# Optimization experiments

Hardware: AMD Instinct MI355X
Metric: run time of the kernel (lower is better)

The kernel has to match this reference:

```python
import jax, jax.numpy as jnp
import numpy as np

HEADS = 2
NEG_SLOPE = 0.2
EPS = 1e-16


def setup_inputs() -> dict:
    N, E, D, F = 10000, 320000, 128, 16
    key = jax.random.key(0)
    ks = jax.random.split(key, 8)
    return {
        "x": jax.random.normal(ks[0], (N, D), dtype=jnp.float32),
        "edge_index": jax.random.randint(ks[1], (2, E), 0, N, dtype=jnp.int64),
        "edge_attr": jax.random.normal(ks[2], (E, F), dtype=jnp.float32),
        # stacked per-layer params (5 layers), glorot-ish scale
        "weights": jax.random.normal(ks[3], (5, D, HEADS * D), dtype=jnp.float32) * 0.08,
        "atts": jax.random.normal(ks[4], (5, HEADS, 2 * D), dtype=jnp.float32) * 0.08,
        "biases": jnp.zeros((5, D), dtype=jnp.float32),
        "edge_ws": jax.random.normal(ks[5], (5, HEADS * D, F), dtype=jnp.float32) * 0.2,
        "edge_bs": jnp.zeros((5, HEADS * D), dtype=jnp.float32),
    }


def _gat_layer(x, src, dst, edge_attr_full, W, att, b, ew, eb):
    # x: [N, D]; src/dst: [E_tot] (self loops already appended)
    N, D = x.shape
    H = HEADS
    edge_emb = edge_attr_full @ ew.T + eb               # [E_tot, H*D]
    xw = x @ W                                          # [N, H*D]
    xj = xw[src].reshape(-1, H, D) + edge_emb.reshape(-1, H, D)  # [E_tot, H, D]
    xi = xw[dst].reshape(-1, H, D)
    att_i, att_j = att[:, :D], att[:, D:]               # [H, D] each
    alpha = jnp.einsum('ehd,hd->eh', xi, att_i) + jnp.einsum('ehd,hd->eh', xj, att_j)
    alpha = jax.nn.leaky_relu(alpha, NEG_SLOPE)
    # segment softmax over destination node (every node has a self loop)
    amax = jax.ops.segment_max(alpha, dst, num_segments=N)   # [N, H]
    ea = jnp.exp(alpha - amax[dst])
    denom = jax.ops.segment_sum(ea, dst, num_segments=N)     # [N, H]
    alpha = ea / (denom[dst] + EPS)
    msg = xj * alpha[..., None]                              # [E_tot, H, D]
    aggr = jax.ops.segment_sum(msg, dst, num_segments=N)     # [N, H, D]
    return aggr.mean(axis=1) + b                             # [N, D]


def reference(x, edge_index, edge_attr, weights, atts, biases, edge_ws, edge_bs):
    N = x.shape[0]
    E = edge_index.shape[1]
    F = edge_attr.shape[1]
    # add self loops (PyG flow: edge_index[0]=source j, edge_index[1]=target i)
    loop = jnp.arange(N, dtype=edge_index.dtype)
    src = jnp.concatenate([edge_index[0], loop])
    dst = jnp.concatenate([edge_index[1], loop])
    edge_attr_full = jnp.concatenate(
        [edge_attr, jnp.zeros((N, F), dtype=edge_attr.dtype)], axis=0)
    h = x
    for l in range(5):
        h = _gat_layer(h, src, dst, edge_attr_full,
                       weights[l], atts[l], biases[l], edge_ws[l], edge_bs[l])
        if l < 4:
            h = jax.nn.relu(h)
    return h
```

## Files before the change

### kernel.cpp

```cpp
#include <hip/hip_runtime.h>
#include <hip/hip_fp16.h>
#include <hip/hip_fp8.h>

#define HEADS 2
#define DD 128
#define FF 16
#define HD 256
#define NEG_SLOPE 0.2f
#define EPSV 1e-16f
#define BB 8

typedef float v2f __attribute__((ext_vector_type(2)));

static __device__ __forceinline__ float rdlanef(float v, int i){
  return __uint_as_float(__builtin_amdgcn_readlane(__float_as_uint(v), i));
}
static __device__ __forceinline__ int rdlanei(int v, int i){
  return __builtin_amdgcn_readlane(v, i);
}
static __device__ __forceinline__ float4 h4f(uint2 u){
  float2 f0 = __half22float2(*(__half2*)&u.x);
  float2 f1 = __half22float2(*(__half2*)&u.y);
  return make_float4(f0.x, f0.y, f1.x, f1.y);
}
static __device__ __forceinline__ float4 fp8x4_to_f4(unsigned u){
#if __has_builtin(__builtin_amdgcn_cvt_pk_f32_fp8)
  v2f lo = __builtin_amdgcn_cvt_pk_f32_fp8(u, false);
  v2f hi = __builtin_amdgcn_cvt_pk_f32_fp8(u, true);
  return make_float4(lo.x, lo.y, hi.x, hi.y);
#else
  __hip_fp8_e4m3 b0, b1, b2, b3;
  b0.__x = (unsigned char)(u & 0xff);
  b1.__x = (unsigned char)((u >> 8) & 0xff);
  b2.__x = (unsigned char)((u >> 16) & 0xff);
  b3.__x = (unsigned char)((u >> 24) & 0xff);
  return make_float4((float)b0, (float)b1, (float)b2, (float)b3);
#endif
}

__global__ void k_hist_prec(const int* __restrict__ dst, int* __restrict__ counts,
                            const float* __restrict__ atts, const float* __restrict__ edge_ws,
                            const float* __restrict__ edge_bs, const float* __restrict__ weights,
                            float* __restrict__ c5, __half* __restrict__ wh,
                            int E, int Etot, int ebl){
  int bid = blockIdx.x;
  if (bid >= ebl){
    int k = bid - ebl;
    if (k < 5){
      int l = k, t = threadIdx.x;
      const float* att = atts    + (size_t)l*HEADS*2*DD;
      const float* ew  = edge_ws + (size_t)l*HD*FF;
      const float* eb  = edge_bs + (size_t)l*HD;
      float* c = c5 + (size_t)l*34;
      if (t < 32){
        int h = t >> 4, f = t & 15;
        float acc = 0.f;
        for (int d = 0; d < DD; d++) acc += att[h*2*DD + DD + d]*ew[(size_t)(h*DD+d)*FF + f];
        c[h*FF + f] = acc;
      } else if (t < 34){
        int h = t - 32;
        float acc = 0.f;
        for (int d = 0; d < DD; d++) acc += att[h*2*DD + DD + d]*eb[h*DD + d];
        c[32 + h] = acc;
      }
    } else {
      int base = (k - 5)*1024 + threadIdx.x*4;
      float4 w = *(const float4*)&weights[base];
      __half2 p0 = __floats2half2_rn(w.x, w.y);
      __half2 p1 = __floats2half2_rn(w.z, w.w);
      uint2 pk; pk.x = *(unsigned*)&p0; pk.y = *(unsigned*)&p1;
      *(uint2*)&wh[base] = pk;
    }
    return;
  }
  int e = bid*256 + threadIdx.x;
  if (e >= Etot) return;
  int dn = (e < E) ? dst[e] : (e - E);
  atomicAdd(&counts[dn], 1);
}

__global__ __launch_bounds__(1024) void k_scan(const int* __restrict__ counts, int* __restrict__ starts,
                       int* __restrict__ cursor, int N, int Etot){
  __shared__ int s[1024];
  int t = threadIdx.x;
  const int CHN = (N + 1023) / 1024;
  int lo = t*CHN, hi = min(lo+CHN, N);
  int loc = 0;
  for (int i = lo; i < hi; i++) loc += counts[i];
  s[t] = loc;
  __syncthreads();
  for (int off = 1; off < 1024; off <<= 1){
    int v = (t >= off) ? s[t-off] : 0;
    __syncthreads();
    s[t] += v;
    __syncthreads();
  }
  int run = (t == 0) ? 0 : s[t-1];
  for (int i = lo; i < hi; i++){
    starts[i] = run; cursor[i] = run; run += counts[i];
  }
  if (t == 0) starts[N] = Etot;
}

__global__ void k_scatter(const int* __restrict__ dst, int* __restrict__ cursor,
                          int* __restrict__ eids, int E, int Etot){
  int e = blockIdx.x*256 + threadIdx.x;
  if (e >= Etot) return;
  int dn = (e < E) ? dst[e] : (e - E);
  int pos = atomicAdd(&cursor[dn], 1);
  eids[pos] = e;
}

__global__ void k_gather_csr(const int* __restrict__ eids, const int* __restrict__ src,
                             const float* __restrict__ eattr, const float* __restrict__ c5,
                             int* __restrict__ srcC, __half* __restrict__ attrC16,
                             float* __restrict__ attrdot, int E, int Etot){
  int i = blockIdx.x*256 + threadIdx.x;
  if (i >= Etot) return;
  int eid = eids[i];
  float a[FF];
  if (eid < E){
    srcC[i] = src[eid];
    const float4* in = (const float4*)&eattr[(size_t)eid*FF];
    float4 q0=in[0], q1=in[1], q2=in[2], q3=in[3];
    a[0]=q0.x; a[1]=q0.y; a[2]=q0.z; a[3]=q0.w;
    a[4]=q1.x; a[5]=q1.y; a[6]=q1.z; a[7]=q1.w;
    a[8]=q2.x; a[9]=q2.y; a[10]=q2.z; a[11]=q2.w;
    a[12]=q3.x; a[13]=q3.y; a[14]=q3.z; a[15]=q3.w;
  } else {
    srcC[i] = eid - E;
    #pragma unroll
    for (int f = 0; f < FF; f++) a[f] = 0.f;
  }
  uint4 pk0, pk1;
  {
    __half2 h0 = __floats2half2_rn(a[0],a[1]),  h1 = __floats2half2_rn(a[2],a[3]);
    __half2 h2 = __floats2half2_rn(a[4],a[5]),  h3 = __floats2half2_rn(a[6],a[7]);
    __half2 h4 = __floats2half2_rn(a[8],a[9]),  h5 = __floats2half2_rn(a[10],a[11]);
    __half2 h6 = __floats2half2_rn(a[12],a[13]),h7 = __floats2half2_rn(a[14],a[15]);
    pk0.x=*(unsigned*)&h0; pk0.y=*(unsigned*)&h1; pk0.z=*(unsigned*)&h2; pk0.w=*(unsigned*)&h3;
    pk1.x=*(unsigned*)&h4; pk1.y=*(unsigned*)&h5; pk1.z=*(unsigned*)&h6; pk1.w=*(unsigned*)&h7;
  }
  uint4* ob = (uint4*)&attrC16[(size_t)i*FF];
  ob[0] = pk0; ob[1] = pk1;
  #pragma unroll
  for (int l = 0; l < 5; l++){
    const float* cl = c5 + (size_t)l*34;
    float d0 = 0.f, d1 = 0.f;
    #pragma unroll
    for (int f = 0; f < FF; f++){
      d0 = fmaf(a[f], cl[f], d0);
      d1 = fmaf(a[f], cl[FF+f], d1);
    }
    *(float2*)&attrdot[((size_t)l*Etot + i)*2] = make_float2(d0, d1);
  }
}

__global__ __launch_bounds__(256) void k_gemm_xw(const float* __restrict__ h, const __half* __restrict__ Wh,
                         const float* __restrict__ att, unsigned char* __restrict__ xw8,
                         float* __restrict__ sbuf, int N){
  __shared__ float sx[16][DD];
  int r0 = blockIdx.x * 16;
  int rows = min(16, N - r0);
  int t = threadIdx.x;
  for (int idx = t; idx < 16*(DD/4); idx += 256){
    int r = idx >> 5, kq = idx & 31;
    float4 v = make_float4(0.f,0.f,0.f,0.f);
    if (r < rows) v = *(const float4*)&h[(size_t)(r0+r)*DD + kq*4];
    *(float4*)&sx[r][kq*4] = v;
  }
  __syncthreads();
  int tx = t & 63, ty = t >> 6;
  int c0 = tx*4;
  float4 acc[4];
  #pragma unroll
  for (int r = 0; r < 4; r++) acc[r] = make_float4(0.f,0.f,0.f,0.f);
  #pragma unroll 4
  for (int kq = 0; kq < 32; kq++){
    float4 w0 = h4f(*(const uint2*)&Wh[(size_t)(kq*4+0)*HD + c0]);
    float4 w1 = h4f(*(const uint2*)&Wh[(size_t)(kq*4+1)*HD + c0]);
    float4 w2 = h4f(*(const uint2*)&Wh[(size_t)(kq*4+2)*HD + c0]);
    float4 w3 = h4f(*(const uint2*)&Wh[(size_t)(kq*4+3)*HD + c0]);
    #pragma unroll
    for (int r = 0; r < 4; r++){
      float4 hv = *(const float4*)&sx[ty*4+r][kq*4];
      acc[r].x = fmaf(hv.x, w0.x, acc[r].x); acc[r].y = fmaf(hv.x, w0.y, acc[r].y);
      acc[r].z = fmaf(hv.x, w0.z, acc[r].z); acc[r].w = fmaf(hv.x, w0.w, acc[r].w);
      acc[r].x = fmaf(hv.y, w1.x, acc[r].x); acc[r].y = fmaf(hv.y, w1.y, acc[r].y);
      acc[r].z = fmaf(hv.y, w1.z, acc[r].z); acc[r].w = fmaf(hv.y, w1.w, acc[r].w);
      acc[r].x = fmaf(hv.z, w2.x, acc[r].x); acc[r].y = fmaf(hv.z, w2.y, acc[r].y);
      acc[r].z = fmaf(hv.z, w2.z, acc[r].z); acc[r].w = fmaf(hv.z, w2.w, acc[r].w);
      acc[r].x = fmaf(hv.w, w3.x, acc[r].x); acc[r].y = fmaf(hv.w, w3.y, acc[r].y);
      acc[r].z = fmaf(hv.w, w3.z, acc[r].z); acc[r].w = fmaf(hv.w, w3.w, acc[r].w);
    }
  }
  #pragma unroll
  for (int r = 0; r < 4; r++){
    if (ty*4+r < rows){
      __hip_fp8_e4m3 q0(acc[r].x), q1(acc[r].y), q2(acc[r].z), q3(acc[r].w);
      unsigned pk = (unsigned)q0.__x | ((unsigned)q1.__x << 8)
                  | ((unsigned)q2.__x << 16) | ((unsigned)q3.__x << 24);
      *(unsigned*)&xw8[(size_t)(r0+ty*4+r)*HD + c0] = pk;
    }
  }
  int hsel = tx >> 5;
  int cm = c0 & 127;
  float4 ai = *(const float4*)&att[hsel*2*DD + cm];
  float4 aj = *(const float4*)&att[hsel*2*DD + DD + cm];
  #pragma unroll
  for (int r = 0; r < 4; r++){
    float pi = acc[r].x*ai.x + acc[r].y*ai.y + acc[r].z*ai.z + acc[r].w*ai.w;
    float pj = acc[r].x*aj.x + acc[r].y*aj.y + acc[r].z*aj.z + acc[r].w*aj.w;
    #pragma unroll
    for (int off = 16; off; off >>= 1){
      pi += __shfl_xor(pi, off);
      pj += __shfl_xor(pj, off);
    }
    int row = ty*4 + r;
    if ((tx & 31) == 0 && row < rows){
      sbuf[(size_t)(r0+row)*4 + 0 + hsel] = pi;
      sbuf[(size_t)(r0+row)*4 + 2 + hsel] = pj;
    }
  }
}

__global__ __launch_bounds__(128, 8) void k_aggr(const int* __restrict__ starts, const int* __restrict__ srcC,
                      const __half* __restrict__ attrC16, const float* __restrict__ adL,
                      const float* __restrict__ s, const float* __restrict__ c,
                      const unsigned char* __restrict__ xw8, const float* __restrict__ ew,
                      const float* __restrict__ eb, const float* __restrict__ bias,
                      float* __restrict__ out, int N, int relu){
  int lane = threadIdx.x & 63, wid = threadIdx.x >> 6;
  int n = blockIdx.x*2 + wid;
  if (n >= N) return;

  float c32 = c[32], c33 = c[33];
  float sdx = s[(size_t)n*4+0], sdy = s[(size_t)n*4+1];
  int st = starts[n];
  int deg = starts[n+1] - st;

  int f2 = lane & 15;
  int h2 = (lane >> 4) & 1;
  int hq = lane >> 5;
  const unsigned char* xbase = xw8 + lane*4;

  float aAx=0.f, aAy=0.f, aAz=0.f, aAw=0.f;
  float aBx=0.f, aBy=0.f, aBz=0.f, aBw=0.f;
  float ls0=0.f, ls1=0.f, taccA=0.f, taccB=0.f;

  for (int base = 0; base < deg; base += 64){
    int cnt = min(64, deg - base);
    float e0 = 0.f, e1 = 0.f; int msrc = 0;
    if (lane < cnt){
      int idx = st + base + lane;
      msrc = srcC[idx];
      float2 sj = *(const float2*)&s[(size_t)msrc*4+2];
      float2 ad = *(const float2*)&adL[(size_t)idx*2];
      float x0 = sdx + sj.x + c32 + ad.x;
      float x1 = sdy + sj.y + c33 + ad.y;
      x0 = (x0 > 0.f) ? x0 : NEG_SLOPE*x0;
      x1 = (x1 > 0.f) ? x1 : NEG_SLOPE*x1;
      e0 = expf(x0); e1 = expf(x1);
      ls0 += e0; ls1 += e1;
    }
    const __half* abase = &attrC16[(size_t)(st+base)*FF + f2];
    int i = 0;
    for (; i + BB <= cnt; i += BB){
      unsigned u[BB];
      float av[BB];
      #pragma unroll
      for (int k = 0; k < BB; k++){
        int sn = rdlanei(msrc, i+k);
        u[k] = *(const unsigned*)(xbase + (size_t)sn*HD);
      }
      #pragma unroll
      for (int k = 0; k < BB; k++) av[k] = __half2float(abase[(size_t)(i+k)*FF]);
      #pragma unroll
      for (int k = 0; k < BB; k++){
        float w0 = rdlanef(e0, i+k);
        float w1 = rdlanef(e1, i+k);
        float ws = hq ? w1 : w0;
        float wt = h2 ? w1 : w0;
        float4 xv = fp8x4_to_f4(u[k]);
        if (k & 1){
          aBx = fmaf(ws, xv.x, aBx); aBy = fmaf(ws, xv.y, aBy);
          aBz = fmaf(ws, xv.z, aBz); aBw = fmaf(ws, xv.w, aBw);
          taccB = fmaf(wt, av[k], taccB);
        } else {
          aAx = fmaf(ws, xv.x, aAx); aAy = fmaf(ws, xv.y, aAy);
          aAz = fmaf(ws, xv.z, aAz); aAw = fmaf(ws, xv.w, aAw);
          taccA = fmaf(wt, av[k], taccA);
        }
      }
    }
    for (; i < cnt; i++){
      int sn = rdlanei(msrc, i);
      float w0 = rdlanef(e0, i);
      float w1 = rdlanef(e1, i);
      unsigned u0 = *(const unsigned*)(xbase + (size_t)sn*HD);
      float av0 = __half2float(abase[(size_t)i*FF]);
      float ws = hq ? w1 : w0;
      float wt = h2 ? w1 : w0;
      float4 xv = fp8x4_to_f4(u0);
      aAx = fmaf(ws, xv.x, aAx); aAy = fmaf(ws, xv.y, aAy);
      aAz = fmaf(ws, xv.z, aAz); aAw = fmaf(ws, xv.w, aAw);
      taccA = fmaf(wt, av0, taccA);
    }
  }
  float ax = aAx + aBx, ay = aAy + aBy, az = aAz + aBz, aw = aAw + aBw;
  float tacc = taccA + taccB;
  #pragma unroll
  for (int off = 32; off; off >>= 1){
    ls0 += __shfl_xor(ls0, off);
    ls1 += __shfl_xor(ls1, off);
  }

  int c0 = lane*4;
  float th[FF];
  #pragma unroll
  for (int f = 0; f < FF; f++) th[f] = __shfl(tacc, hq*FF + f);
  float embq[4];
  #pragma unroll
  for (int q = 0; q < 4; q++){
    const float4* er = (const float4*)&ew[(size_t)(c0+q)*FF];
    float4 g0 = er[0], g1 = er[1], g2 = er[2], g3 = er[3];
    float v = th[0]*g0.x + th[1]*g0.y + th[2]*g0.z + th[3]*g0.w;
    v = fmaf(th[4],  g1.x, v); v = fmaf(th[5],  g1.y, v); v = fmaf(th[6],  g1.z, v); v = fmaf(th[7],  g1.w, v);
    v = fmaf(th[8],  g2.x, v); v = fmaf(th[9],  g2.y, v); v = fmaf(th[10], g2.z, v); v = fmaf(th[11], g2.w, v);
    v = fmaf(th[12], g3.x, v); v = fmaf(th[13], g3.y, v); v = fmaf(th[14], g3.z, v); v = fmaf(th[15], g3.w, v);
    embq[q] = v;
  }
  float di = 1.f/((hq ? ls1 : ls0) + EPSV);
  float4 ebv = *(const float4*)&eb[c0];
  float r0 = di*(ax + embq[0]) + ebv.x;
  float r1 = di*(ay + embq[1]) + ebv.y;
  float r2 = di*(az + embq[2]) + ebv.z;
  float r3 = di*(aw + embq[3]) + ebv.w;
  float p0 = __shfl_xor(r0, 32);
  float p1 = __shfl_xor(r1, 32);
  float p2 = __shfl_xor(r2, 32);
  float p3 = __shfl_xor(r3, 32);
  if (lane < 32){
    float4 bv = *(const float4*)&bias[c0];
    float4 v;
    v.x = 0.5f*(r0 + p0) + bv.x;
    v.y = 0.5f*(r1 + p1) + bv.y;
    v.z = 0.5f*(r2 + p2) + bv.z;
    v.w = 0.5f*(r3 + p3) + bv.w;
    if (relu){
      v.x = fmaxf(v.x, 0.f); v.y = fmaxf(v.y, 0.f);
      v.z = fmaxf(v.z, 0.f); v.w = fmaxf(v.w, 0.f);
    }
    *(float4*)&out[(size_t)n*DD + c0] = v;
  }
}

extern "C" void kernel_launch(void* const* d_in, const int* in_sizes, int n_in,
                              void* d_out, int out_size, void* d_ws, size_t ws_size,
                              hipStream_t stream){
  const float* x       = (const float*)d_in[0];
  const int*   eidx    = (const int*)d_in[1];
  const float* eattr   = (const float*)d_in[2];
  const float* weights = (const float*)d_in[3];
  const float* atts    = (const float*)d_in[4];
  const float* biases  = (const float*)d_in[5];
  const float* edge_ws = (const float*)d_in[6];
  const float* edge_bs = (const float*)d_in[7];
  const int N = in_sizes[0]/DD;
  const int E = in_sizes[1]/2;
  const int Etot = E + N;
  const int* src = eidx;
  const int* dst = eidx + E;

  char* p = (char*)d_ws;
  auto alloc = [&](size_t bytes){ void* r = (void*)p; p += (bytes + 255) & ~(size_t)255; return r; };
  float*         hA      = (float*)alloc((size_t)N*DD*4);
  float*         hB      = (float*)alloc((size_t)N*DD*4);
  unsigned char* xw8     = (unsigned char*)alloc((size_t)N*HD);
  float*         sbuf    = (float*)alloc((size_t)N*4*4);
  int*           starts  = (int*)alloc((size_t)(N+1)*4);
  int*           srcC    = (int*)alloc((size_t)Etot*4);
  int*           eids    = (int*)alloc((size_t)Etot*4);
  __half*        attrC16 = (__half*)alloc((size_t)Etot*FF*2);
  float*         attrdot = (float*)alloc((size_t)5*Etot*2*4);
  __half*        wh      = (__half*)alloc((size_t)5*DD*HD*2);
  float*         c5      = (float*)alloc(5*34*4);

  int* counts = (int*)sbuf;
  int* cursor = (int*)((char*)sbuf + 65536);

  const int ebl = (Etot + 255)/256;

  (void)hipMemsetAsync(counts, 0, (size_t)N*4, stream);
  k_hist_prec<<<ebl+165, 256, 0, stream>>>(dst, counts, atts, edge_ws, edge_bs, weights,
                                           c5, wh, E, Etot, ebl);
  k_scan<<<1, 1024, 0, stream>>>(counts, starts, cursor, N, Etot);
  k_scatter<<<ebl, 256, 0, stream>>>(dst, cursor, eids, E, Etot);
  k_gather_csr<<<ebl, 256, 0, stream>>>(eids, src, eattr, c5, srcC, attrC16, attrdot, E, Etot);

  const float* hin = x;
  for (int l = 0; l < 5; l++){
    const __half* Whl = wh + (size_t)l*DD*HD;
    const float* att = atts    + (size_t)l*HEADS*2*DD;
    const float* b   = biases  + (size_t)l*DD;
    const float* ew  = edge_ws + (size_t)l*HD*FF;
    const float* eb  = edge_bs + (size_t)l*HD;
    const float* c   = c5 + (size_t)l*34;
    const float* adL = attrdot + (size_t)l*Etot*2;
    float* hout = (l == 4) ? (float*)d_out : ((l & 1) ? hB : hA);
    int relu = (l < 4) ? 1 : 0;

    k_gemm_xw<<<(N+15)/16, 256, 0, stream>>>(hin, Whl, att, xw8, sbuf, N);
    k_aggr<<<(N+1)/2, 128, 0, stream>>>(starts, srcC, attrC16, adL, sbuf, c, xw8, ew, eb, b, hout, N, relu);

    hin = hout;
  }
}
```

Baseline: 367.8 us.

## Sort nodes by descending degree for aggregation load balancing, 4 waves per block

Adds a degree histogram, scan and scatter pass that builds a node permutation ordered by descending in-degree, and the aggregation kernel now processes nodes in that order. The intent is to group similar-degree nodes within a block and schedule the heaviest nodes first, reducing tail imbalance. Blocks grow from 2 to 4 waves and the occupancy hint is dropped. It costs three small extra kernels and a memset, and permuted node order scatters output writes and reads of per-node data.

```diff
diff --git a/kernel.cpp b/kernel.cpp
--- a/kernel.cpp
+++ b/kernel.cpp
@@ -9,6 +9,7 @@
 #define NEG_SLOPE 0.2f
 #define EPSV 1e-16f
 #define BB 8
+#define DBINS 1024
 
 typedef float v2f __attribute__((ext_vector_type(2)));
 
@@ -111,6 +112,36 @@
   eids[pos] = e;
 }
 
+__global__ void k_dhist(const int* __restrict__ starts, int* __restrict__ dhist, int N){
+  int n = blockIdx.x*256 + threadIdx.x;
+  if (n >= N) return;
+  int d = min(starts[n+1] - starts[n], DBINS-1);
+  atomicAdd(&dhist[d], 1);
+}
+__global__ __launch_bounds__(1024) void k_dscan(const int* __restrict__ dhist, int* __restrict__ dcur){
+  __shared__ int s[DBINS];
+  int t = threadIdx.x;
+  s[t] = dhist[DBINS-1-t];
+  __syncthreads();
+  for (int off = 1; off < DBINS; off <<= 1){
+    int v = (t >= off) ? s[t-off] : 0;
+    __syncthreads();
+    s[t] += v;
+    __syncthreads();
+  }
+  int incl = s[t];
+  int excl = incl - dhist[DBINS-1-t];
+  dcur[DBINS-1-t] = excl;
+}
+__global__ void k_dscatter(const int* __restrict__ starts, int* __restrict__ dcur,
+                           int* __restrict__ perm, int N){
+  int n = blockIdx.x*256 + threadIdx.x;
+  if (n >= N) return;
+  int d = min(starts[n+1] - starts[n], DBINS-1);
+  int pos = atomicAdd(&dcur[d], 1);
+  perm[pos] = n;
+}
+
 __global__ void k_gather_csr(const int* __restrict__ eids, const int* __restrict__ src,
                              const float* __restrict__ eattr, const float* __restrict__ c5,
                              int* __restrict__ srcC, __half* __restrict__ attrC16,
@@ -224,15 +255,17 @@
   }
 }
 
-__global__ __launch_bounds__(128, 8) void k_aggr(const int* __restrict__ starts, const int* __restrict__ srcC,
+__global__ __launch_bounds__(256) void k_aggr(const int* __restrict__ perm,
+                      const int* __restrict__ starts, const int* __restrict__ srcC,
                       const __half* __restrict__ attrC16, const float* __restrict__ adL,
                       const float* __restrict__ s, const float* __restrict__ c,
                       const unsigned char* __restrict__ xw8, const float* __restrict__ ew,
                       const float* __restrict__ eb, const float* __restrict__ bias,
                       float* __restrict__ out, int N, int relu){
   int lane = threadIdx.x & 63, wid = threadIdx.x >> 6;
-  int n = blockIdx.x*2 + wid;
-  if (n >= N) return;
+  int ni = blockIdx.x*4 + wid;
+  if (ni >= N) return;
+  int n = perm[ni];
 
   float c32 = c[32], c33 = c[33];
   float sdx = s[(size_t)n*4+0], sdy = s[(size_t)n*4+1];
@@ -385,17 +418,25 @@
   float*         attrdot = (float*)alloc((size_t)5*Etot*2*4);
   __half*        wh      = (__half*)alloc((size_t)5*DD*HD*2);
   float*         c5      = (float*)alloc(5*34*4);
+  int*           perm    = (int*)alloc((size_t)N*4);
+  int*           dhist   = (int*)alloc((size_t)DBINS*4);
+  int*           dcur    = (int*)alloc((size_t)DBINS*4);
 
   int* counts = (int*)sbuf;
   int* cursor = (int*)((char*)sbuf + 65536);
 
   const int ebl = (Etot + 255)/256;
+  const int nbl = (N + 255)/256;
 
   (void)hipMemsetAsync(counts, 0, (size_t)N*4, stream);
+  (void)hipMemsetAsync(dhist, 0, (size_t)DBINS*4, stream);
   k_hist_prec<<<ebl+165, 256, 0, stream>>>(dst, counts, atts, edge_ws, edge_bs, weights,
                                            c5, wh, E, Etot, ebl);
   k_scan<<<1, 1024, 0, stream>>>(counts, starts, cursor, N, Etot);
   k_scatter<<<ebl, 256, 0, stream>>>(dst, cursor, eids, E, Etot);
+  k_dhist<<<nbl, 256, 0, stream>>>(starts, dhist, N);
+  k_dscan<<<1, DBINS, 0, stream>>>(dhist, dcur);
+  k_dscatter<<<nbl, 256, 0, stream>>>(starts, dcur, perm, N);
   k_gather_csr<<<ebl, 256, 0, stream>>>(eids, src, eattr, c5, srcC, attrC16, attrdot, E, Etot);
 
   const float* hin = x;
@@ -411,7 +452,7 @@
     int relu = (l < 4) ? 1 : 0;
 
     k_gemm_xw<<<(N+15)/16, 256, 0, stream>>>(hin, Whl, att, xw8, sbuf, N);
-    k_aggr<<<(N+1)/2, 128, 0, stream>>>(starts, srcC, attrC16, adL, sbuf, c, xw8, ew, eb, b, hout, N, relu);
+    k_aggr<<<(N+3)/4, 256, 0, stream>>>(perm, starts, srcC, attrC16, adL, sbuf, c, xw8, ew, eb, b, hout, N, relu);
 
     hin = hout;
   }
```

New measurement: 401.0 us. 1.09x slower.
